# Optimization experiments

Measured on AMD Instinct MI355X. Metric: run time of the kernel, lower is better.

## Reference

```python
import jax, jax.numpy as jnp
import numpy as np

N_NODES = 100000
N_EDGES = 1600000
IN_FEATS = 256
OUT_FEATS = 128


def setup_inputs() -> dict:
    key = jax.random.key(0)
    k1, k2, k3, k4, k5 = jax.random.split(key, 5)
    feat = jax.random.normal(k1, (N_NODES, IN_FEATS), dtype=jnp.float32)
    # xavier_uniform-like init for the weight
    limit = float(np.sqrt(6.0 / (IN_FEATS + OUT_FEATS)))
    weight = jax.random.uniform(k2, (IN_FEATS, OUT_FEATS), dtype=jnp.float32,
                                minval=-limit, maxval=limit)
    edge_weight = jax.random.uniform(k3, (N_EDGES,), dtype=jnp.float32)
    src = jax.random.randint(k4, (N_EDGES,), 0, N_NODES, dtype=jnp.int64)
    dst = jax.random.randint(k5, (N_EDGES,), 0, N_NODES, dtype=jnp.int64)
    return {"feat": feat, "weight": weight, "edge_weight": edge_weight,
            "src": src, "dst": dst}


def reference(feat, weight, edge_weight, src, dst):
    N = feat.shape[0]
    ones = jnp.ones(src.shape, dtype=feat.dtype)
    # out/in degrees from edge list (clamped to >= 1), as in DGL
    out_deg = jnp.clip(jax.ops.segment_sum(ones, src, num_segments=N), 1.0)
    in_deg = jnp.clip(jax.ops.segment_sum(ones, dst, num_segments=N), 1.0)
    # norm == 'both': pre-scale sources by out_deg^-0.5
    feat_src = feat * (out_deg ** -0.5)[:, None]
    # in_feats > out_feats branch: transform (with tanh) BEFORE aggregation
    h = jnp.tanh(feat_src @ weight)                      # [N, out]
    # message = u_mul_e: h[src] * edge_weight, then sum per destination
    m = h[src] * edge_weight[:, None]                    # [E, out]
    rst = jax.ops.segment_sum(m, dst, num_segments=N)    # [N, out]
    # norm == 'both': post-scale by in_deg^-0.5
    rst = rst * (in_deg ** -0.5)[:, None]
    return rst
```

## Files before the change

kernel.cpp:

```cpp
#include <hip/hip_runtime.h>
#include <hip/hip_fp16.h>
#include <math.h>

#define N_NODES 100000
#define N_EDGES 1600000
#define IN_F 256
#define OUT_F 128
#define SCAN_TPB 256
#define SCAN_EPB 1024

#define HR 4
#define HRANGE 25000
#define HC 64
#define HCHUNK 25000
#define PWORDS (N_NODES / 2)

#define GM_ROWS 64
#define BK 32

typedef _Float16 h8 __attribute__((ext_vector_type(8)));
typedef float f4 __attribute__((ext_vector_type(4)));

#define GLD16(gp, lp) __builtin_amdgcn_global_load_lds( \
    (const __attribute__((address_space(1))) unsigned int*)(gp), \
    (__attribute__((address_space(3))) unsigned int*)(lp), 16, 0, 0)

__global__ __launch_bounds__(256) void hist_kernel(
        const int* __restrict__ src, const int* __restrict__ dst,
        int* __restrict__ rank, unsigned int* __restrict__ partial_in,
        unsigned int* __restrict__ partial_out) {
    __shared__ unsigned int bins[HRANGE / 2];
    int b = blockIdx.x;
    int c = b >> 3;
    int tr = b & 7;
    int type = tr >> 2;
    int r = tr & 3;
    for (int i = threadIdx.x; i < HRANGE / 2; i += 256) bins[i] = 0;
    __syncthreads();
    const int* nodes = type ? src : dst;
    const int e0 = c * HCHUNK;
    const int lo = r * HRANGE;
    const int ngroups = HCHUNK / 4;
    for (int g = threadIdx.x; g < ngroups; g += 256) {
        int e = e0 + g * 4;
        int4 n4 = *(const int4*)(nodes + e);
        int nn[4] = {n4.x, n4.y, n4.z, n4.w};
        #pragma unroll
        for (int j = 0; j < 4; ++j) {
            unsigned loc = (unsigned)(nn[j] - lo);
            if (loc < (unsigned)HRANGE) {
                unsigned sh = (loc & 1) * 16;
                unsigned old = atomicAdd(&bins[loc >> 1], 1u << sh);
                if (type == 0) rank[e + j] = (int)((old >> sh) & 0xffffu);
            }
        }
    }
    __syncthreads();
    unsigned int* part = type ? partial_out : partial_in;
    unsigned int* dstp = part + (size_t)c * PWORDS + (lo >> 1);
    for (int i = threadIdx.x; i < HRANGE / 2; i += 256) dstp[i] = bins[i];
}

__global__ __launch_bounds__(256) void fused_reduce_kernel(
        const unsigned int* __restrict__ partial_in,
        const unsigned int* __restrict__ partial_out,
        unsigned short* __restrict__ chunk_base16,
        int* __restrict__ deg_in, float* __restrict__ rs_out,
        int* __restrict__ spart, int N) {
    __shared__ int tmp[256];
    int t = threadIdx.x;
    int n0 = blockIdx.x * SCAN_EPB + t * 4;
    int run[4] = {0, 0, 0, 0};
    int sout[4] = {0, 0, 0, 0};
    if (n0 < N) {
        const int w0 = n0 >> 1;
        #pragma unroll 4
        for (int c = 0; c < HC; ++c) {
            ushort4 cb;
            cb.x = (unsigned short)run[0]; cb.y = (unsigned short)run[1];
            cb.z = (unsigned short)run[2]; cb.w = (unsigned short)run[3];
            *(ushort4*)(chunk_base16 + (size_t)c * N_NODES + n0) = cb;
            uint2 pi = *(const uint2*)(partial_in + (size_t)c * PWORDS + w0);
            run[0] += (int)(pi.x & 0xffffu);  run[1] += (int)(pi.x >> 16);
            run[2] += (int)(pi.y & 0xffffu);  run[3] += (int)(pi.y >> 16);
            uint2 po = *(const uint2*)(partial_out + (size_t)c * PWORDS + w0);
            sout[0] += (int)(po.x & 0xffffu); sout[1] += (int)(po.x >> 16);
            sout[2] += (int)(po.y & 0xffffu); sout[3] += (int)(po.y >> 16);
        }
        *(int4*)(deg_in + n0) = make_int4(run[0], run[1], run[2], run[3]);
        float4 rs;
        rs.x = rsqrtf((float)(sout[0] < 1 ? 1 : sout[0]));
        rs.y = rsqrtf((float)(sout[1] < 1 ? 1 : sout[1]));
        rs.z = rsqrtf((float)(sout[2] < 1 ? 1 : sout[2]));
        rs.w = rsqrtf((float)(sout[3] < 1 ? 1 : sout[3]));
        *(float4*)(rs_out + n0) = rs;
    }
    tmp[t] = run[0] + run[1] + run[2] + run[3];
    __syncthreads();
    for (int off = 128; off > 0; off >>= 1) {
        if (t < off) tmp[t] += tmp[t + off];
        __syncthreads();
    }
    if (t == 0) spart[blockIdx.x] = tmp[0];
}

__global__ __launch_bounds__(128) void scan_part2(const int* __restrict__ partials,
                                                  int* __restrict__ bases, int nb) {
    __shared__ int tmp[128];
    int t = threadIdx.x;
    int v = (t < nb) ? partials[t] : 0;
    tmp[t] = v;
    __syncthreads();
    int x = v;
    for (int off = 1; off < 128; off <<= 1) {
        int y = (t >= off) ? tmp[t - off] : 0;
        __syncthreads();
        x += y;
        tmp[t] = x;
        __syncthreads();
    }
    if (t < nb) bases[t] = x - v;
}

__global__ __launch_bounds__(SCAN_TPB) void scan_part3(const int* __restrict__ deg,
                                                       const int* __restrict__ bases,
                                                       int* __restrict__ row_ptr, int N) {
    __shared__ int tmp[SCAN_TPB];
    int t = threadIdx.x;
    int i0 = blockIdx.x * SCAN_EPB + t * 4;
    int v[4];
    int s = 0;
    #pragma unroll
    for (int j = 0; j < 4; ++j) { v[j] = (i0 + j < N) ? deg[i0 + j] : 0; s += v[j]; }
    tmp[t] = s;
    __syncthreads();
    int x = s;
    for (int off = 1; off < SCAN_TPB; off <<= 1) {
        int y = (t >= off) ? tmp[t - off] : 0;
        __syncthreads();
        x += y;
        tmp[t] = x;
        __syncthreads();
    }
    int excl = bases[blockIdx.x] + x - s;
    #pragma unroll
    for (int j = 0; j < 4; ++j) {
        if (i0 + j < N) row_ptr[i0 + j] = excl;
        excl += v[j];
    }
    if (blockIdx.x == gridDim.x - 1 && t == SCAN_TPB - 1) row_ptr[N] = bases[blockIdx.x] + x;
}

__global__ __launch_bounds__(256) void fill_kernel(
        const int* __restrict__ src, const int* __restrict__ dst,
        const float* __restrict__ ew, const int* __restrict__ row_ptr,
        const unsigned short* __restrict__ chunk_base16,
        const int* __restrict__ rank, int2* __restrict__ ed, int E) {
    int e0 = (blockIdx.x * 256 + threadIdx.x) * 4;
    if (e0 >= E) return;
    int4 s4 = *(const int4*)(src + e0);
    int4 d4 = *(const int4*)(dst + e0);
    float4 w4 = *(const float4*)(ew + e0);
    int4 r4 = *(const int4*)(rank + e0);
    int c = e0 / HCHUNK;
    const unsigned short* cb = chunk_base16 + (size_t)c * N_NODES;
    int dd[4] = {d4.x, d4.y, d4.z, d4.w};
    int ss[4] = {s4.x, s4.y, s4.z, s4.w};
    int rr[4] = {r4.x, r4.y, r4.z, r4.w};
    float ww[4] = {w4.x, w4.y, w4.z, w4.w};
    #pragma unroll
    for (int j = 0; j < 4; ++j) {
        int d = dd[j];
        int p = row_ptr[d] + (int)cb[d] + rr[j];
        unsigned long long v = (unsigned long long)(unsigned int)ss[j] |
                               ((unsigned long long)(unsigned int)__float_as_int(ww[j]) << 32);
        __builtin_nontemporal_store(v, (unsigned long long*)&ed[p]);
    }
}

__global__ void wt_kernel(const float* __restrict__ W, _Float16* __restrict__ Wt) {
    int i = blockIdx.x * blockDim.x + threadIdx.x;
    if (i < IN_F * OUT_F) {
        int n = i >> 8;
        int k = i & 255;
        Wt[i] = (_Float16)W[k * OUT_F + n];
    }
}

__device__ __forceinline__ float fast_tanh(float x) {
    float e = __expf(2.0f * x);
    return 1.0f - 2.0f / (e + 1.0f);
}

__global__ __launch_bounds__(256, 4) void gemm_mfma_kernel(
        const float* __restrict__ feat, const _Float16* __restrict__ Wt,
        const float* __restrict__ rs_out, __half* __restrict__ h, int N) {
    __shared__ float    a_lds[2][GM_ROWS * BK];
    __shared__ _Float16 b_lds[2][OUT_F * BK];

    const int tid  = threadIdx.x;
    const int wave = tid >> 6;
    const int lane = tid & 63;
    const int m    = lane & 15;
    const int quad = lane >> 4;
    const int n0   = wave * 32;
    const int r0   = blockIdx.x * GM_ROWS;

    const int l3 = lane >> 3;
    const int ag = (lane & 7) ^ l3;
    int arow0 = r0 + 16 * wave + l3;      if (arow0 >= N) arow0 = N - 1;
    int arow1 = r0 + 16 * wave + 8 + l3;  if (arow1 >= N) arow1 = N - 1;
    const float* ga0 = feat + (size_t)arow0 * IN_F + ag * 4;
    const float* ga1 = feat + (size_t)arow1 * IN_F + ag * 4;
    const int brow0 = 32 * wave + (lane >> 2);
    const int brow1 = 32 * wave + 16 + (lane >> 2);
    const _Float16* gb0 = Wt + (size_t)brow0 * IN_F + (lane & 3) * 8;
    const _Float16* gb1 = Wt + (size_t)brow1 * IN_F + (lane & 3) * 8;

    f4 acc[4][2];
    #pragma unroll
    for (int t = 0; t < 4; ++t) {
        acc[t][0] = (f4){0.f, 0.f, 0.f, 0.f};
        acc[t][1] = (f4){0.f, 0.f, 0.f, 0.f};
    }

    GLD16(ga0, &a_lds[0][(16 * wave) * BK]);
    GLD16(ga1, &a_lds[0][(16 * wave + 8) * BK]);
    GLD16(gb0, &b_lds[0][(32 * wave) * BK]);
    GLD16(gb1, &b_lds[0][(32 * wave + 16) * BK]);
    __syncthreads();

    #pragma unroll
    for (int kt = 0; kt < IN_F / BK; ++kt) {
        const int cb = kt & 1;
        if (kt < IN_F / BK - 1) {
            const int nb2 = cb ^ 1;
            const int ko = (kt + 1) * BK;
            GLD16(ga0 + ko, &a_lds[nb2][(16 * wave) * BK]);
            GLD16(ga1 + ko, &a_lds[nb2][(16 * wave + 8) * BK]);
            GLD16(gb0 + ko, &b_lds[nb2][(32 * wave) * BK]);
            GLD16(gb1 + ko, &b_lds[nb2][(32 * wave + 16) * BK]);
            __builtin_amdgcn_sched_barrier(0);
        }
        h8 b0 = *(const h8*)&b_lds[cb][(n0 + m) * BK + quad * 8];
        h8 b1 = *(const h8*)&b_lds[cb][(n0 + 16 + m) * BK + quad * 8];
        #pragma unroll
        for (int t = 0; t < 4; ++t) {
            const int ar = t * 16 + m;
            float4 alo = *(const float4*)&a_lds[cb][ar * BK + (((quad * 2)     ^ (m & 7)) * 4)];
            float4 ahi = *(const float4*)&a_lds[cb][ar * BK + (((quad * 2 + 1) ^ (m & 7)) * 4)];
            h8 a;
            a[0] = (_Float16)alo.x; a[1] = (_Float16)alo.y;
            a[2] = (_Float16)alo.z; a[3] = (_Float16)alo.w;
            a[4] = (_Float16)ahi.x; a[5] = (_Float16)ahi.y;
            a[6] = (_Float16)ahi.z; a[7] = (_Float16)ahi.w;
            acc[t][0] = __builtin_amdgcn_mfma_f32_16x16x32_f16(a, b0, acc[t][0], 0, 0, 0);
            acc[t][1] = __builtin_amdgcn_mfma_f32_16x16x32_f16(a, b1, acc[t][1], 0, 0, 0);
        }
        __syncthreads();
    }

    #pragma unroll
    for (int t = 0; t < 4; ++t) {
        const int crow = r0 + t * 16 + quad * 4;
        float4 rs4 = *(const float4*)&rs_out[crow];
        const float rsv[4] = {rs4.x, rs4.y, rs4.z, rs4.w};
        #pragma unroll
        for (int r = 0; r < 4; ++r) {
            const int rr = crow + r;
            if (rr < N) {
                h[(size_t)rr * OUT_F + n0 + m]      = __float2half(fast_tanh(acc[t][0][r] * rsv[r]));
                h[(size_t)rr * OUT_F + n0 + 16 + m] = __float2half(fast_tanh(acc[t][1][r] * rsv[r]));
            }
        }
    }
}

__global__ __launch_bounds__(256) void gather_kernel(
        const __half* __restrict__ h, const int2* __restrict__ ed,
        const int* __restrict__ row_ptr, float* __restrict__ out, int N) {
    int wave = threadIdx.x >> 6;
    int lane = threadIdx.x & 63;
    int node = blockIdx.x * 4 + wave;
    if (node >= N) return;
    int lo = row_ptr[node];
    int hi = row_ptr[node + 1];
    int p = lane >> 4;
    int c = lane & 15;
    float acc[4][8];
    #pragma unroll
    for (int g = 0; g < 4; ++g)
        #pragma unroll
        for (int i = 0; i < 8; ++i) acc[g][i] = 0.f;

    for (int j = lo; j < hi; j += 16) {
        #pragma unroll
        for (int g = 0; g < 4; ++g) {
            int jj = j + g * 4 + p;
            int2 e = (jj < hi) ? ed[jj] : make_int2(0, 0);
            float w = __int_as_float(e.y);
            int4 rrow = *(const int4*)(h + (size_t)e.x * OUT_F + c * 8);
            float2 t;
            t = __half22float2(*(__half2*)&rrow.x); acc[g][0] += w * t.x; acc[g][1] += w * t.y;
            t = __half22float2(*(__half2*)&rrow.y); acc[g][2] += w * t.x; acc[g][3] += w * t.y;
            t = __half22float2(*(__half2*)&rrow.z); acc[g][4] += w * t.x; acc[g][5] += w * t.y;
            t = __half22float2(*(__half2*)&rrow.w); acc[g][6] += w * t.x; acc[g][7] += w * t.y;
        }
    }
    float v[8];
    #pragma unroll
    for (int i = 0; i < 8; ++i) {
        v[i] = (acc[0][i] + acc[1][i]) + (acc[2][i] + acc[3][i]);
        v[i] += __shfl_xor(v[i], 16);
        v[i] += __shfl_xor(v[i], 32);
    }
    if (p == 0) {
        int deg = hi - lo; if (deg < 1) deg = 1;
        float rs = rsqrtf((float)deg);
        float* op = out + (size_t)node * OUT_F + c * 8;
        *(float4*)op       = make_float4(v[0] * rs, v[1] * rs, v[2] * rs, v[3] * rs);
        *(float4*)(op + 4) = make_float4(v[4] * rs, v[5] * rs, v[6] * rs, v[7] * rs);
    }
}

extern "C" void kernel_launch(void* const* d_in, const int* in_sizes, int n_in,
                              void* d_out, int out_size, void* d_ws, size_t ws_size,
                              hipStream_t stream) {
    const float* feat   = (const float*)d_in[0];
    const float* weight = (const float*)d_in[1];
    const float* ew     = (const float*)d_in[2];
    const int*   src    = (const int*)d_in[3];
    const int*   dst    = (const int*)d_in[4];
    float* out = (float*)d_out;

    char* ws = (char*)d_ws;
    float* rs_out      = (float*)(ws);
    int*   deg_in      = (int*)(ws + 400000);
    int*   row_ptr     = (int*)(ws + 800000);
    int*   spart       = (int*)(ws + 1200016);
    int*   sbases      = (int*)(ws + 1200528);
    int*   rank        = (int*)(ws + 1201056);
    unsigned int* partial_in  = (unsigned int*)(ws + 7601056);
    int2*  ed          = (int2*)(ws + 7601056);
    unsigned short* chunk_base16 = (unsigned short*)(ws + 20401056);
    unsigned int* partial_out = (unsigned int*)(ws + 33201056);
    __half* h          = (__half*)(ws + 20401056);
    _Float16* Wt       = (_Float16*)(ws + 46001056);

    const int nb = (N_NODES + SCAN_EPB - 1) / SCAN_EPB;

    hist_kernel<<<2 * HR * HC, 256, 0, stream>>>(src, dst, rank, partial_in, partial_out);
    fused_reduce_kernel<<<nb, 256, 0, stream>>>(partial_in, partial_out, chunk_base16,
                                                deg_in, rs_out, spart, N_NODES);
    scan_part2<<<1, 128, 0, stream>>>(spart, sbases, nb);
    scan_part3<<<nb, SCAN_TPB, 0, stream>>>(deg_in, sbases, row_ptr, N_NODES);
    fill_kernel<<<(N_EDGES / 4 + 255) / 256, 256, 0, stream>>>(src, dst, ew, row_ptr,
                                                               chunk_base16, rank, ed, N_EDGES);
    wt_kernel<<<(IN_F * OUT_F + 255) / 256, 256, 0, stream>>>(weight, Wt);
    gemm_mfma_kernel<<<(N_NODES + GM_ROWS - 1) / GM_ROWS, 256, 0, stream>>>(feat, Wt, rs_out, h, N_NODES);
    gather_kernel<<<(N_NODES + 3) / 4, 256, 0, stream>>>(h, ed, row_ptr, out, N_NODES);
}
```

Before: 377.2 us.

## Replace shared-memory chunked histogram CSR build with global atomic counting and cursor fill

```diff
diff --git a/kernel.cpp b/kernel.cpp
--- a/kernel.cpp
+++ b/kernel.cpp
@@ -9,93 +9,60 @@
 #define SCAN_TPB 256
 #define SCAN_EPB 1024
 
-#define HR 4
-#define HRANGE 25000
-#define HC 64
-#define HCHUNK 25000
-#define PWORDS (N_NODES / 2)
-
 #define GM_ROWS 64
 #define BK 32
 
 typedef _Float16 h8 __attribute__((ext_vector_type(8)));
 typedef float f4 __attribute__((ext_vector_type(4)));
+typedef int   i4v __attribute__((ext_vector_type(4)));
+typedef float f4v __attribute__((ext_vector_type(4)));
 
 #define GLD16(gp, lp) __builtin_amdgcn_global_load_lds( \
     (const __attribute__((address_space(1))) unsigned int*)(gp), \
     (__attribute__((address_space(3))) unsigned int*)(lp), 16, 0, 0)
 
-__global__ __launch_bounds__(256) void hist_kernel(
+__global__ __launch_bounds__(256) void zero_kernel(int4* __restrict__ deg_in4,
+                                                   int4* __restrict__ deg_out4) {
+    int i = blockIdx.x * 256 + threadIdx.x;
+    if (i < N_NODES / 4) {
+        deg_in4[i]  = make_int4(0, 0, 0, 0);
+        deg_out4[i] = make_int4(0, 0, 0, 0);
+    }
+}
+
+__global__ __launch_bounds__(256) void count_kernel(
         const int* __restrict__ src, const int* __restrict__ dst,
-        int* __restrict__ rank, unsigned int* __restrict__ partial_in,
-        unsigned int* __restrict__ partial_out) {
-    __shared__ unsigned int bins[HRANGE / 2];
-    int b = blockIdx.x;
-    int c = b >> 3;
-    int tr = b & 7;
-    int type = tr >> 2;
-    int r = tr & 3;
-    for (int i = threadIdx.x; i < HRANGE / 2; i += 256) bins[i] = 0;
-    __syncthreads();
-    const int* nodes = type ? src : dst;
-    const int e0 = c * HCHUNK;
-    const int lo = r * HRANGE;
-    const int ngroups = HCHUNK / 4;
-    for (int g = threadIdx.x; g < ngroups; g += 256) {
-        int e = e0 + g * 4;
-        int4 n4 = *(const int4*)(nodes + e);
-        int nn[4] = {n4.x, n4.y, n4.z, n4.w};
-        #pragma unroll
-        for (int j = 0; j < 4; ++j) {
-            unsigned loc = (unsigned)(nn[j] - lo);
-            if (loc < (unsigned)HRANGE) {
-                unsigned sh = (loc & 1) * 16;
-                unsigned old = atomicAdd(&bins[loc >> 1], 1u << sh);
-                if (type == 0) rank[e + j] = (int)((old >> sh) & 0xffffu);
-            }
-        }
-    }
-    __syncthreads();
-    unsigned int* part = type ? partial_out : partial_in;
-    unsigned int* dstp = part + (size_t)c * PWORDS + (lo >> 1);
-    for (int i = threadIdx.x; i < HRANGE / 2; i += 256) dstp[i] = bins[i];
-}
-
-__global__ __launch_bounds__(256) void fused_reduce_kernel(
-        const unsigned int* __restrict__ partial_in,
-        const unsigned int* __restrict__ partial_out,
-        unsigned short* __restrict__ chunk_base16,
-        int* __restrict__ deg_in, float* __restrict__ rs_out,
-        int* __restrict__ spart, int N) {
+        int* __restrict__ deg_out, int* __restrict__ deg_in, int E) {
+    int e0 = (blockIdx.x * 256 + threadIdx.x) * 4;
+    if (e0 >= E) return;
+    i4v s4 = __builtin_nontemporal_load((const i4v*)(src + e0));
+    i4v d4 = __builtin_nontemporal_load((const i4v*)(dst + e0));
+    #pragma unroll
+    for (int j = 0; j < 4; ++j) {
+        atomicAdd(&deg_out[s4[j]], 1);
+        atomicAdd(&deg_in[d4[j]], 1);
+    }
+}
+
+__global__ __launch_bounds__(256) void deg_pass_kernel(
+        const int* __restrict__ deg_in, const int* __restrict__ deg_out,
+        float* __restrict__ rs_out, int* __restrict__ spart, int N) {
     __shared__ int tmp[256];
     int t = threadIdx.x;
     int n0 = blockIdx.x * SCAN_EPB + t * 4;
-    int run[4] = {0, 0, 0, 0};
-    int sout[4] = {0, 0, 0, 0};
+    int s = 0;
     if (n0 < N) {
-        const int w0 = n0 >> 1;
-        #pragma unroll 4
-        for (int c = 0; c < HC; ++c) {
-            ushort4 cb;
-            cb.x = (unsigned short)run[0]; cb.y = (unsigned short)run[1];
-            cb.z = (unsigned short)run[2]; cb.w = (unsigned short)run[3];
-            *(ushort4*)(chunk_base16 + (size_t)c * N_NODES + n0) = cb;
-            uint2 pi = *(const uint2*)(partial_in + (size_t)c * PWORDS + w0);
-            run[0] += (int)(pi.x & 0xffffu);  run[1] += (int)(pi.x >> 16);
-            run[2] += (int)(pi.y & 0xffffu);  run[3] += (int)(pi.y >> 16);
-            uint2 po = *(const uint2*)(partial_out + (size_t)c * PWORDS + w0);
-            sout[0] += (int)(po.x & 0xffffu); sout[1] += (int)(po.x >> 16);
-            sout[2] += (int)(po.y & 0xffffu); sout[3] += (int)(po.y >> 16);
-        }
-        *(int4*)(deg_in + n0) = make_int4(run[0], run[1], run[2], run[3]);
+        int4 di = *(const int4*)(deg_in + n0);
+        s = di.x + di.y + di.z + di.w;
+        int4 dq = *(const int4*)(deg_out + n0);
         float4 rs;
-        rs.x = rsqrtf((float)(sout[0] < 1 ? 1 : sout[0]));
-        rs.y = rsqrtf((float)(sout[1] < 1 ? 1 : sout[1]));
-        rs.z = rsqrtf((float)(sout[2] < 1 ? 1 : sout[2]));
-        rs.w = rsqrtf((float)(sout[3] < 1 ? 1 : sout[3]));
+        rs.x = rsqrtf((float)(dq.x < 1 ? 1 : dq.x));
+        rs.y = rsqrtf((float)(dq.y < 1 ? 1 : dq.y));
+        rs.z = rsqrtf((float)(dq.z < 1 ? 1 : dq.z));
+        rs.w = rsqrtf((float)(dq.w < 1 ? 1 : dq.w));
         *(float4*)(rs_out + n0) = rs;
     }
-    tmp[t] = run[0] + run[1] + run[2] + run[3];
+    tmp[t] = s;
     __syncthreads();
     for (int off = 128; off > 0; off >>= 1) {
         if (t < off) tmp[t] += tmp[t + off];
@@ -124,7 +91,8 @@
 
 __global__ __launch_bounds__(SCAN_TPB) void scan_part3(const int* __restrict__ deg,
                                                        const int* __restrict__ bases,
-                                                       int* __restrict__ row_ptr, int N) {
+                                                       int* __restrict__ row_ptr,
+                                                       int* __restrict__ cursor, int N) {
     __shared__ int tmp[SCAN_TPB];
     int t = threadIdx.x;
     int i0 = blockIdx.x * SCAN_EPB + t * 4;
@@ -145,7 +113,7 @@
     int excl = bases[blockIdx.x] + x - s;
     #pragma unroll
     for (int j = 0; j < 4; ++j) {
-        if (i0 + j < N) row_ptr[i0 + j] = excl;
+        if (i0 + j < N) { row_ptr[i0 + j] = excl; cursor[i0 + j] = excl; }
         excl += v[j];
     }
     if (blockIdx.x == gridDim.x - 1 && t == SCAN_TPB - 1) row_ptr[N] = bases[blockIdx.x] + x;
@@ -153,27 +121,18 @@
 
 __global__ __launch_bounds__(256) void fill_kernel(
         const int* __restrict__ src, const int* __restrict__ dst,
-        const float* __restrict__ ew, const int* __restrict__ row_ptr,
-        const unsigned short* __restrict__ chunk_base16,
-        const int* __restrict__ rank, int2* __restrict__ ed, int E) {
+        const float* __restrict__ ew, int* __restrict__ cursor,
+        int2* __restrict__ ed, int E) {
     int e0 = (blockIdx.x * 256 + threadIdx.x) * 4;
     if (e0 >= E) return;
-    int4 s4 = *(const int4*)(src + e0);
-    int4 d4 = *(const int4*)(dst + e0);
-    float4 w4 = *(const float4*)(ew + e0);
-    int4 r4 = *(const int4*)(rank + e0);
-    int c = e0 / HCHUNK;
-    const unsigned short* cb = chunk_base16 + (size_t)c * N_NODES;
-    int dd[4] = {d4.x, d4.y, d4.z, d4.w};
-    int ss[4] = {s4.x, s4.y, s4.z, s4.w};
-    int rr[4] = {r4.x, r4.y, r4.z, r4.w};
-    float ww[4] = {w4.x, w4.y, w4.z, w4.w};
+    i4v s4 = __builtin_nontemporal_load((const i4v*)(src + e0));
+    i4v d4 = __builtin_nontemporal_load((const i4v*)(dst + e0));
+    f4v w4 = __builtin_nontemporal_load((const f4v*)(ew + e0));
     #pragma unroll
     for (int j = 0; j < 4; ++j) {
-        int d = dd[j];
-        int p = row_ptr[d] + (int)cb[d] + rr[j];
-        unsigned long long v = (unsigned long long)(unsigned int)ss[j] |
-                               ((unsigned long long)(unsigned int)__float_as_int(ww[j]) << 32);
+        int p = atomicAdd(&cursor[d4[j]], 1);
+        unsigned long long v = (unsigned long long)(unsigned int)s4[j] |
+                               ((unsigned long long)(unsigned int)__float_as_int(w4[j]) << 32);
         __builtin_nontemporal_store(v, (unsigned long long*)&ed[p]);
     }
 }
@@ -339,23 +298,20 @@
     int*   row_ptr     = (int*)(ws + 800000);
     int*   spart       = (int*)(ws + 1200016);
     int*   sbases      = (int*)(ws + 1200528);
-    int*   rank        = (int*)(ws + 1201056);
-    unsigned int* partial_in  = (unsigned int*)(ws + 7601056);
+    int*   deg_out     = (int*)(ws + 1201056);
+    int*   cursor      = (int*)(ws + 1601056);
     int2*  ed          = (int2*)(ws + 7601056);
-    unsigned short* chunk_base16 = (unsigned short*)(ws + 20401056);
-    unsigned int* partial_out = (unsigned int*)(ws + 33201056);
     __half* h          = (__half*)(ws + 20401056);
     _Float16* Wt       = (_Float16*)(ws + 46001056);
 
     const int nb = (N_NODES + SCAN_EPB - 1) / SCAN_EPB;
 
-    hist_kernel<<<2 * HR * HC, 256, 0, stream>>>(src, dst, rank, partial_in, partial_out);
-    fused_reduce_kernel<<<nb, 256, 0, stream>>>(partial_in, partial_out, chunk_base16,
-                                                deg_in, rs_out, spart, N_NODES);
+    zero_kernel<<<(N_NODES / 4 + 255) / 256, 256, 0, stream>>>((int4*)deg_in, (int4*)deg_out);
+    count_kernel<<<(N_EDGES / 4 + 255) / 256, 256, 0, stream>>>(src, dst, deg_out, deg_in, N_EDGES);
+    deg_pass_kernel<<<nb, 256, 0, stream>>>(deg_in, deg_out, rs_out, spart, N_NODES);
     scan_part2<<<1, 128, 0, stream>>>(spart, sbases, nb);
-    scan_part3<<<nb, SCAN_TPB, 0, stream>>>(deg_in, sbases, row_ptr, N_NODES);
-    fill_kernel<<<(N_EDGES / 4 + 255) / 256, 256, 0, stream>>>(src, dst, ew, row_ptr,
-                                                               chunk_base16, rank, ed, N_EDGES);
+    scan_part3<<<nb, SCAN_TPB, 0, stream>>>(deg_in, sbases, row_ptr, cursor, N_NODES);
+    fill_kernel<<<(N_EDGES / 4 + 255) / 256, 256, 0, stream>>>(src, dst, ew, cursor, ed, N_EDGES);
     wt_kernel<<<(IN_F * OUT_F + 255) / 256, 256, 0, stream>>>(weight, Wt);
     gemm_mfma_kernel<<<(N_NODES + GM_ROWS - 1) / GM_ROWS, 256, 0, stream>>>(feat, Wt, rs_out, h, N_NODES);
     gather_kernel<<<(N_NODES + 3) / 4, 256, 0, stream>>>(h, ed, row_ptr, out, N_NODES);
```

After: 528.6 us. +40.1%, slower.
